# Kernel tuning notes

Measured on AMD Instinct MI355X. Metric: run time of the kernel, lower is better.

Reference implementation:

```python
import jax, jax.numpy as jnp
import numpy as np

K_NEIGHBOURS = 40  # includes self; self is dropped after top-k


def setup_inputs() -> dict:
    key = jax.random.key(0)
    ks = jax.random.split(key, 4)
    B, V, F_in = 4, 4096, 64
    P, S, F_out = 64, 4, 64
    x = jax.random.normal(ks[0], (B, V, F_in), dtype=jnp.float32)
    Wf = jax.random.normal(ks[1], (F_in, P), dtype=jnp.float32) / np.sqrt(F_in)
    bf = jnp.zeros((P,), dtype=jnp.float32)
    Ws = jax.random.normal(ks[2], (F_in, S), dtype=jnp.float32) / np.sqrt(F_in)
    bs = jnp.zeros((S,), dtype=jnp.float32)
    Wo = jax.random.normal(ks[3], (F_in + 2 * P, F_out), dtype=jnp.float32) / np.sqrt(F_in + 2 * P)
    bo = jnpp = jnp.zeros((F_out,), dtype=jnp.float32)
    return {"x": x, "Wf": Wf, "bf": bf, "Ws": Ws, "bs": bs, "Wo": Wo, "bo": bo}


def _euclidean_squared(c):
    # c: [B, V, S] -> [B, V, V] squared pairwise distances
    sq = jnp.sum(c * c, axis=-1)  # [B, V]
    d2 = sq[:, :, None] + sq[:, None, :] - 2.0 * jnp.einsum('bvs,bus->bvu', c, c)
    return d2


def reference(x, Wf, bf, Ws, bs, Wo, bo):
    # learned spatial coordinates and propagated features
    coords = x @ Ws + bs            # [B, V, S]
    feats = x @ Wf + bf             # [B, V, P]

    d2 = _euclidean_squared(coords)                 # [B, V, V]
    neg_vals, idx = jax.lax.top_k(-d2, K_NEIGHBOURS)  # closest first (self at 0)
    nbr_idx = idx[:, :, 1:]                         # [B, V, K-1]
    dist = -neg_vals[:, :, 1:]                      # [B, V, K-1] (>= 0)

    # gauss_of_lin(d * 10) = exp(-|10 d|)
    w = jnp.exp(-jnp.abs(dist * 10.0))              # [B, V, K-1]

    # gather neighbour features per batch: [B, V, K-1, P]
    nf = jax.vmap(lambda f, i: f[i])(feats, nbr_idx)
    nf = nf * w[..., None]

    collected = jnp.concatenate([jnp.max(nf, axis=2), jnp.mean(nf, axis=2)], axis=-1)  # [B, V, 2P]
    updated = jnp.concatenate([x, collected], axis=-1)  # [B, V, F_in + 2P]
    return jnp.tanh(updated @ Wo + bo)
```

## Files before the change

### kernel.cpp

```cpp
#include <hip/hip_runtime.h>
#include <cmath>

#define BB  4
#define VV  4096
#define KK  40
#define FIN 64

typedef float v2f __attribute__((ext_vector_type(2)));

__global__ __launch_bounds__(256) void prep_kernel(
    const float* __restrict__ x, const float* __restrict__ Wf,
    const float* __restrict__ bf, const float* __restrict__ Ws,
    const float* __restrict__ bs,
    float* __restrict__ coords, float* __restrict__ sq,
    float* __restrict__ feats)
{
    int lane = threadIdx.x & 63;
    int wid  = threadIdx.x >> 6;
    int row0 = (blockIdx.x * 4 + wid) * 4;
    const float* xr = x + (size_t)row0 * FIN;

    float rx0 = xr[lane];
    float rx1 = xr[64  + lane];
    float rx2 = xr[128 + lane];
    float rx3 = xr[192 + lane];

    float a0 = 0.f, a1 = 0.f, a2 = 0.f, a3 = 0.f;
    #pragma unroll
    for (int k = 0; k < FIN; ++k) {
        float wf = Wf[k * 64 + lane];
        a0 = fmaf(__uint_as_float(
             __builtin_amdgcn_readlane(__float_as_uint(rx0), k)), wf, a0);
        a1 = fmaf(__uint_as_float(
             __builtin_amdgcn_readlane(__float_as_uint(rx1), k)), wf, a1);
        a2 = fmaf(__uint_as_float(
             __builtin_amdgcn_readlane(__float_as_uint(rx2), k)), wf, a2);
        a3 = fmaf(__uint_as_float(
             __builtin_amdgcn_readlane(__float_as_uint(rx3), k)), wf, a3);
    }
    float bfl = bf[lane];
    feats[(size_t)(row0 + 0) * 64 + lane] = a0 + bfl;
    feats[(size_t)(row0 + 1) * 64 + lane] = a1 + bfl;
    feats[(size_t)(row0 + 2) * 64 + lane] = a2 + bfl;
    feats[(size_t)(row0 + 3) * 64 + lane] = a3 + bfl;

    int r  = lane >> 4;
    int s  = (lane >> 2) & 3;
    int kc = lane & 3;
    const float* xrr = x + (size_t)(row0 + r) * FIN + kc * 16;
    const float* wsr = Ws + kc * 16 * 4 + s;
    float c = 0.f;
    #pragma unroll
    for (int k = 0; k < 16; ++k)
        c = fmaf(xrr[k], wsr[k * 4], c);
    c += __shfl_xor(c, 1, 64);
    c += __shfl_xor(c, 2, 64);
    float val = c + bs[s];
    if ((lane & 3) == 0) coords[(size_t)(row0 + r) * 4 + s] = val;
    float p = val * val;
    p += __shfl_xor(p, 4, 64);
    p += __shfl_xor(p, 8, 64);
    if ((lane & 15) == 0) sq[row0 + r] = p;
}

__device__ __forceinline__ unsigned umed3(unsigned a, unsigned b, unsigned c)
{
    unsigned d;
    asm("v_med3_u32 %0, %1, %2, %3" : "=v"(d) : "v"(a), "v"(b), "v"(c));
    return d;
}

__device__ __forceinline__ int cnt_lt4(unsigned m0, unsigned m1,
                                       unsigned m2, unsigned m3,
                                       unsigned cand)
{
    return (int)__popcll(__ballot(m0 < cand))
         + (int)__popcll(__ballot(m1 < cand))
         + (int)__popcll(__ballot(m2 < cand))
         + (int)__popcll(__ballot(m3 < cand));
}

__device__ __forceinline__ unsigned select_thresh(unsigned m0, unsigned m1,
                                                  unsigned m2, unsigned m3)
{
    unsigned M = 0u;
    #pragma unroll
    for (int bit = 30; bit >= 12; --bit) {
        unsigned cand = M | (1u << bit);
        if (cnt_lt4(m0, m1, m2, m3, cand) <= 39) M = cand;
    }
    unsigned Msel = M | 0xFFFu;
    if (cnt_lt4(m0, m1, m2, m3, M + 4096u) != 40) {
        #pragma unroll
        for (int bit = 11; bit >= 0; --bit) {
            unsigned cand = M | (1u << bit);
            if (cnt_lt4(m0, m1, m2, m3, cand) <= 39) M = cand;
        }
        Msel = M;
    }
    return Msel;
}

__device__ __forceinline__ void compact4(unsigned m0, unsigned m1,
                                         unsigned m2, unsigned m3,
                                         unsigned Msel, uint2* dst)
{
    unsigned mn = m0;
    #pragma unroll
    for (int off = 32; off >= 1; off >>= 1) {
        unsigned o = __shfl_xor(mn, off, 64);
        mn = o < mn ? o : mn;
    }
    int base = 0;
    unsigned kk = m0;
    #pragma unroll
    for (int i = 0; i < 4; ++i) {
        bool pred = (kk <= Msel) && (kk != mn);
        unsigned long long mask = __ballot(pred);
        unsigned pos = (unsigned)base +
            __builtin_amdgcn_mbcnt_hi((unsigned)(mask >> 32),
                __builtin_amdgcn_mbcnt_lo((unsigned)mask, 0u));
        if (pred) {
            float d2a = __uint_as_float(kk & 0xFFFFF000u);
            float w   = __expf(-10.f * d2a);
            dst[pos] = make_uint2((kk & 4095u) << 8, __float_as_uint(w));
        }
        base += (int)__popcll(mask);
        kk = (i == 0) ? m1 : (i == 1) ? m2 : m3;
    }
}

__global__ __launch_bounds__(256) void gravnet_kernel(
    const float* __restrict__ x, const float* __restrict__ coords,
    const float* __restrict__ sq, const float* __restrict__ feats,
    const float* __restrict__ Wo, const float* __restrict__ bo,
    float* __restrict__ out)
{
    int lane = threadIdx.x & 63;
    int w    = threadIdx.x >> 6;
    int quad = w >> 1;
    int half = w & 1;
    int qb   = blockIdx.x * 8 + quad * 4;
    int b    = (blockIdx.x * 8) >> 12;
    int v0   = qb & (VV - 1);

    __shared__ __align__(16) char smem[16384];
    uint4* s_mrg = (uint4*)smem;
    uint2* s_nb  = (uint2*)smem;
    float* s_upd = (float*)(smem + 8 * KK * 8);

    const float4* cb  = (const float4*)(coords + (size_t)b * VV * 4);
    const float*  sqb = sq + (size_t)b * VV;

    float4 cq0 = cb[v0],     cq1 = cb[v0 + 1];
    float4 cq2 = cb[v0 + 2], cq3 = cb[v0 + 3];
    v2f nxA = (v2f){-2.f * cq0.x, -2.f * cq1.x};
    v2f nyA = (v2f){-2.f * cq0.y, -2.f * cq1.y};
    v2f nzA = (v2f){-2.f * cq0.z, -2.f * cq1.z};
    v2f nwA = (v2f){-2.f * cq0.w, -2.f * cq1.w};
    v2f hsA = (v2f){sqb[v0], sqb[v0 + 1]};
    v2f nxB = (v2f){-2.f * cq2.x, -2.f * cq3.x};
    v2f nyB = (v2f){-2.f * cq2.y, -2.f * cq3.y};
    v2f nzB = (v2f){-2.f * cq2.z, -2.f * cq3.z};
    v2f nwB = (v2f){-2.f * cq2.w, -2.f * cq3.w};
    v2f hsB = (v2f){sqb[v0 + 2], sqb[v0 + 3]};

    unsigned k00 = ~0u, k01 = ~0u, k02 = ~0u, k03 = ~0u;
    unsigned k10 = ~0u, k11 = ~0u, k12 = ~0u, k13 = ~0u;
    unsigned k20 = ~0u, k21 = ~0u, k22 = ~0u, k23 = ~0u;
    unsigned k30 = ~0u, k31 = ~0u, k32 = ~0u, k33 = ~0u;

    int i0 = half * 32;
    #pragma unroll 4
    for (int i = i0; i < i0 + 32; ++i) {
        int u = i * 64 + lane;
        float4 cu = cb[u];
        float squ = sqb[u];
        v2f accA = hsA + (v2f){squ, squ};
        accA = __builtin_elementwise_fma(nxA, (v2f){cu.x, cu.x}, accA);
        accA = __builtin_elementwise_fma(nyA, (v2f){cu.y, cu.y}, accA);
        accA = __builtin_elementwise_fma(nzA, (v2f){cu.z, cu.z}, accA);
        accA = __builtin_elementwise_fma(nwA, (v2f){cu.w, cu.w}, accA);
        v2f accB = hsB + (v2f){squ, squ};
        accB = __builtin_elementwise_fma(nxB, (v2f){cu.x, cu.x}, accB);
        accB = __builtin_elementwise_fma(nyB, (v2f){cu.y, cu.y}, accB);
        accB = __builtin_elementwise_fma(nzB, (v2f){cu.z, cu.z}, accB);
        accB = __builtin_elementwise_fma(nwB, (v2f){cu.w, cu.w}, accB);

        {
            float d2 = fmaxf(accA.x, 0.f);
            unsigned k = (__float_as_uint(d2) & 0xFFFFF000u) | (unsigned)u;
            unsigned n1 = umed3(k00, k01, k);
            unsigned n2 = umed3(k01, k02, k);
            unsigned n3 = umed3(k02, k03, k);
            k00 = min(k00, k); k01 = n1; k02 = n2; k03 = n3;
        }
        {
            float d2 = fmaxf(accA.y, 0.f);
            unsigned k = (__float_as_uint(d2) & 0xFFFFF000u) | (unsigned)u;
            unsigned n1 = umed3(k10, k11, k);
            unsigned n2 = umed3(k11, k12, k);
            unsigned n3 = umed3(k12, k13, k);
            k10 = min(k10, k); k11 = n1; k12 = n2; k13 = n3;
        }
        {
            float d2 = fmaxf(accB.x, 0.f);
            unsigned k = (__float_as_uint(d2) & 0xFFFFF000u) | (unsigned)u;
            unsigned n1 = umed3(k20, k21, k);
            unsigned n2 = umed3(k21, k22, k);
            unsigned n3 = umed3(k22, k23, k);
            k20 = min(k20, k); k21 = n1; k22 = n2; k23 = n3;
        }
        {
            float d2 = fmaxf(accB.y, 0.f);
            unsigned k = (__float_as_uint(d2) & 0xFFFFF000u) | (unsigned)u;
            unsigned n1 = umed3(k30, k31, k);
            unsigned n2 = umed3(k31, k32, k);
            unsigned n3 = umed3(k32, k33, k);
            k30 = min(k30, k); k31 = n1; k32 = n2; k33 = n3;
        }
    }

    s_mrg[(w * 4 + 0) * 64 + lane] = make_uint4(k00, k01, k02, k03);
    s_mrg[(w * 4 + 1) * 64 + lane] = make_uint4(k10, k11, k12, k13);
    s_mrg[(w * 4 + 2) * 64 + lane] = make_uint4(k20, k21, k22, k23);
    s_mrg[(w * 4 + 3) * 64 + lane] = make_uint4(k30, k31, k32, k33);
    __syncthreads();

    int p   = w ^ 1;
    int lq0 = half * 2;
    uint4 pb0 = s_mrg[(p * 4 + lq0)     * 64 + lane];
    uint4 pb1 = s_mrg[(p * 4 + lq0 + 1) * 64 + lane];
    unsigned oa0 = half ? k20 : k00, oa1 = half ? k21 : k01;
    unsigned oa2 = half ? k22 : k02, oa3 = half ? k23 : k03;
    unsigned ob0 = half ? k30 : k10, ob1 = half ? k31 : k11;
    unsigned ob2 = half ? k32 : k12, ob3 = half ? k33 : k13;
    __syncthreads();

    unsigned d0 = min(oa0, pb0.w), d1 = min(oa1, pb0.z);
    unsigned d2 = min(oa2, pb0.y), d3 = min(oa3, pb0.x);
    unsigned A0 = min(d0, d3), A3 = max(d0, d3);
    unsigned e0 = min(ob0, pb1.w), e1 = min(ob1, pb1.z);
    unsigned e2 = min(ob2, pb1.y), e3 = min(ob3, pb1.x);
    unsigned B0 = min(e0, e3), B3 = max(e0, e3);

    int s0 = w * 2, s1 = w * 2 + 1;
    compact4(A0, d1, d2, A3, select_thresh(A0, d1, d2, A3), &s_nb[s0 * KK]);
    compact4(B0, e1, e2, B3, select_thresh(B0, e1, e2, B3), &s_nb[s1 * KK]);

    const float* fb  = feats + (size_t)b * VV * 64;
    const char*  fbl = (const char*)(fb + lane);
    float vmax0 = -INFINITY, vsum0 = 0.f, vmax1 = -INFINITY, vsum1 = 0.f;
    #pragma unroll 6
    for (int j = 0; j < KK - 1; ++j) {
        uint2 n0 = s_nb[s0 * KK + j];
        uint2 n1 = s_nb[s1 * KK + j];
        float f0 = *(const float*)(fbl + n0.x);
        float f1 = *(const float*)(fbl + n1.x);
        float g0 = __uint_as_float(n0.y) * f0;
        float g1 = __uint_as_float(n1.y) * f1;
        vmax0 = fmaxf(vmax0, g0); vsum0 += g0;
        vmax1 = fmaxf(vmax1, g1); vsum1 += g1;
    }

    int q0g = qb + lq0, q1g = qb + lq0 + 1;
    s_upd[s0 * 192 + lane]       = x[(size_t)q0g * 64 + lane];
    s_upd[s0 * 192 + 64  + lane] = vmax0;
    s_upd[s0 * 192 + 128 + lane] = vsum0 * (1.0f / 39.0f);
    s_upd[s1 * 192 + lane]       = x[(size_t)q1g * 64 + lane];
    s_upd[s1 * 192 + 64  + lane] = vmax1;
    s_upd[s1 * 192 + 128 + lane] = vsum1 * (1.0f / 39.0f);

    float bol = bo[lane];
    float acc0 = bol, acc1 = bol;
    #pragma unroll 4
    for (int j4 = 0; j4 < 48; ++j4) {
        float wo0 = Wo[(j4 * 4 + 0) * 64 + lane];
        float wo1 = Wo[(j4 * 4 + 1) * 64 + lane];
        float wo2 = Wo[(j4 * 4 + 2) * 64 + lane];
        float wo3 = Wo[(j4 * 4 + 3) * 64 + lane];
        float4 u0 = *(const float4*)&s_upd[s0 * 192 + j4 * 4];
        float4 u1 = *(const float4*)&s_upd[s1 * 192 + j4 * 4];
        acc0 = fmaf(u0.x, wo0, acc0);  acc1 = fmaf(u1.x, wo0, acc1);
        acc0 = fmaf(u0.y, wo1, acc0);  acc1 = fmaf(u1.y, wo1, acc1);
        acc0 = fmaf(u0.z, wo2, acc0);  acc1 = fmaf(u1.z, wo2, acc1);
        acc0 = fmaf(u0.w, wo3, acc0);  acc1 = fmaf(u1.w, wo3, acc1);
    }
    float e0t = __expf(2.f * acc0);
    float e1t = __expf(2.f * acc1);
    out[(size_t)q0g * 64 + lane] = 1.f - __fdividef(2.f, e0t + 1.f);
    out[(size_t)q1g * 64 + lane] = 1.f - __fdividef(2.f, e1t + 1.f);
}

extern "C" void kernel_launch(void* const* d_in, const int* in_sizes, int n_in,
                              void* d_out, int out_size, void* d_ws, size_t ws_size,
                              hipStream_t stream)
{
    (void)in_sizes; (void)n_in; (void)out_size; (void)ws_size;
    const float* x  = (const float*)d_in[0];
    const float* Wf = (const float*)d_in[1];
    const float* bf = (const float*)d_in[2];
    const float* Ws = (const float*)d_in[3];
    const float* bs = (const float*)d_in[4];
    const float* Wo = (const float*)d_in[5];
    const float* bo = (const float*)d_in[6];
    float* out = (float*)d_out;

    float* coords = (float*)d_ws;
    float* sq     = coords + (size_t)BB * VV * 4;
    float* feats  = sq + (size_t)BB * VV;

    prep_kernel<<<BB * VV / 16, 256, 0, stream>>>(x, Wf, bf, Ws, bs,
                                                  coords, sq, feats);
    gravnet_kernel<<<BB * VV / 8, 256, 0, stream>>>(x, coords, sq, feats,
                                                    Wo, bo, out);
}
```

Before: 119.9 us.

## Swizzle block order, use v_bfi keys, and pack aggregation/output matmul into v2f

Remaps blockIdx so consecutive blocks are spread across batch/vertex ranges with an XCD-style stride of eight. Builds the distance|index sort key with a single v_bfi_b32 instead of an and/or pair. Vectorises the neighbour max/sum and the output projection into packed two-lane float math, storing the x/max/mean inputs interleaved per query pair so one float4 LDS read feeds two packed FMAs. These changes aim to cut VALU instruction count and improve cache locality, at the cost of extra register packing and a changed LDS layout.

```diff
diff --git a/kernel.cpp b/kernel.cpp
--- a/kernel.cpp
+++ b/kernel.cpp
@@ -70,6 +70,14 @@
     return d;
 }
 
+__device__ __forceinline__ unsigned bfi_key(unsigned maskv, unsigned d2b,
+                                            unsigned u)
+{
+    unsigned d;
+    asm("v_bfi_b32 %0, %1, %2, %3" : "=v"(d) : "v"(maskv), "v"(d2b), "v"(u));
+    return d;
+}
+
 __device__ __forceinline__ int cnt_lt4(unsigned m0, unsigned m1,
                                        unsigned m2, unsigned m3,
                                        unsigned cand)
@@ -140,8 +148,9 @@
     int w    = threadIdx.x >> 6;
     int quad = w >> 1;
     int half = w & 1;
-    int qb   = blockIdx.x * 8 + quad * 4;
-    int b    = (blockIdx.x * 8) >> 12;
+    int bid  = (int)((blockIdx.x & 7) * 256 + (blockIdx.x >> 3));
+    int qb   = bid * 8 + quad * 4;
+    int b    = (bid * 8) >> 12;
     int v0   = qb & (VV - 1);
 
     __shared__ __align__(16) char smem[16384];
@@ -169,6 +178,8 @@
     unsigned k10 = ~0u, k11 = ~0u, k12 = ~0u, k13 = ~0u;
     unsigned k20 = ~0u, k21 = ~0u, k22 = ~0u, k23 = ~0u;
     unsigned k30 = ~0u, k31 = ~0u, k32 = ~0u, k33 = ~0u;
+
+    unsigned maskv = 0xFFFFF000u;
 
     int i0 = half * 32;
     #pragma unroll 4
@@ -189,7 +200,7 @@
 
         {
             float d2 = fmaxf(accA.x, 0.f);
-            unsigned k = (__float_as_uint(d2) & 0xFFFFF000u) | (unsigned)u;
+            unsigned k = bfi_key(maskv, __float_as_uint(d2), (unsigned)u);
             unsigned n1 = umed3(k00, k01, k);
             unsigned n2 = umed3(k01, k02, k);
             unsigned n3 = umed3(k02, k03, k);
@@ -197,7 +208,7 @@
         }
         {
             float d2 = fmaxf(accA.y, 0.f);
-            unsigned k = (__float_as_uint(d2) & 0xFFFFF000u) | (unsigned)u;
+            unsigned k = bfi_key(maskv, __float_as_uint(d2), (unsigned)u);
             unsigned n1 = umed3(k10, k11, k);
             unsigned n2 = umed3(k11, k12, k);
             unsigned n3 = umed3(k12, k13, k);
@@ -205,7 +216,7 @@
         }
         {
             float d2 = fmaxf(accB.x, 0.f);
-            unsigned k = (__float_as_uint(d2) & 0xFFFFF000u) | (unsigned)u;
+            unsigned k = bfi_key(maskv, __float_as_uint(d2), (unsigned)u);
             unsigned n1 = umed3(k20, k21, k);
             unsigned n2 = umed3(k21, k22, k);
             unsigned n3 = umed3(k22, k23, k);
@@ -213,7 +224,7 @@
         }
         {
             float d2 = fmaxf(accB.y, 0.f);
-            unsigned k = (__float_as_uint(d2) & 0xFFFFF000u) | (unsigned)u;
+            unsigned k = bfi_key(maskv, __float_as_uint(d2), (unsigned)u);
             unsigned n1 = umed3(k30, k31, k);
             unsigned n2 = umed3(k31, k32, k);
             unsigned n3 = umed3(k32, k33, k);
@@ -250,44 +261,42 @@
 
     const float* fb  = feats + (size_t)b * VV * 64;
     const char*  fbl = (const char*)(fb + lane);
-    float vmax0 = -INFINITY, vsum0 = 0.f, vmax1 = -INFINITY, vsum1 = 0.f;
+    v2f vmax01 = (v2f){-INFINITY, -INFINITY};
+    v2f vsum01 = (v2f){0.f, 0.f};
     #pragma unroll 6
     for (int j = 0; j < KK - 1; ++j) {
         uint2 n0 = s_nb[s0 * KK + j];
         uint2 n1 = s_nb[s1 * KK + j];
         float f0 = *(const float*)(fbl + n0.x);
         float f1 = *(const float*)(fbl + n1.x);
-        float g0 = __uint_as_float(n0.y) * f0;
-        float g1 = __uint_as_float(n1.y) * f1;
-        vmax0 = fmaxf(vmax0, g0); vsum0 += g0;
-        vmax1 = fmaxf(vmax1, g1); vsum1 += g1;
+        v2f g01 = (v2f){f0, f1} *
+                  (v2f){__uint_as_float(n0.y), __uint_as_float(n1.y)};
+        vmax01 = __builtin_elementwise_max(vmax01, g01);
+        vsum01 += g01;
     }
 
     int q0g = qb + lq0, q1g = qb + lq0 + 1;
-    s_upd[s0 * 192 + lane]       = x[(size_t)q0g * 64 + lane];
-    s_upd[s0 * 192 + 64  + lane] = vmax0;
-    s_upd[s0 * 192 + 128 + lane] = vsum0 * (1.0f / 39.0f);
-    s_upd[s1 * 192 + lane]       = x[(size_t)q1g * 64 + lane];
-    s_upd[s1 * 192 + 64  + lane] = vmax1;
-    s_upd[s1 * 192 + 128 + lane] = vsum1 * (1.0f / 39.0f);
+    float* sb = s_upd + w * 384;
+    *(float2*)&sb[lane * 2] =
+        make_float2(x[(size_t)q0g * 64 + lane], x[(size_t)q1g * 64 + lane]);
+    *(float2*)&sb[128 + lane * 2] = make_float2(vmax01.x, vmax01.y);
+    *(float2*)&sb[256 + lane * 2] =
+        make_float2(vsum01.x * (1.0f / 39.0f), vsum01.y * (1.0f / 39.0f));
 
     float bol = bo[lane];
-    float acc0 = bol, acc1 = bol;
-    #pragma unroll 4
-    for (int j4 = 0; j4 < 48; ++j4) {
-        float wo0 = Wo[(j4 * 4 + 0) * 64 + lane];
-        float wo1 = Wo[(j4 * 4 + 1) * 64 + lane];
-        float wo2 = Wo[(j4 * 4 + 2) * 64 + lane];
-        float wo3 = Wo[(j4 * 4 + 3) * 64 + lane];
-        float4 u0 = *(const float4*)&s_upd[s0 * 192 + j4 * 4];
-        float4 u1 = *(const float4*)&s_upd[s1 * 192 + j4 * 4];
-        acc0 = fmaf(u0.x, wo0, acc0);  acc1 = fmaf(u1.x, wo0, acc1);
-        acc0 = fmaf(u0.y, wo1, acc0);  acc1 = fmaf(u1.y, wo1, acc1);
-        acc0 = fmaf(u0.z, wo2, acc0);  acc1 = fmaf(u1.z, wo2, acc1);
-        acc0 = fmaf(u0.w, wo3, acc0);  acc1 = fmaf(u1.w, wo3, acc1);
-    }
-    float e0t = __expf(2.f * acc0);
-    float e1t = __expf(2.f * acc1);
+    v2f acc01 = (v2f){bol, bol};
+    #pragma unroll 8
+    for (int jj = 0; jj < 96; ++jj) {
+        float wo0 = Wo[(jj * 2 + 0) * 64 + lane];
+        float wo1 = Wo[(jj * 2 + 1) * 64 + lane];
+        float4 up = *(const float4*)&sb[jj * 4];
+        acc01 = __builtin_elementwise_fma((v2f){up.x, up.y},
+                                          (v2f){wo0, wo0}, acc01);
+        acc01 = __builtin_elementwise_fma((v2f){up.z, up.w},
+                                          (v2f){wo1, wo1}, acc01);
+    }
+    float e0t = __expf(2.f * acc01.x);
+    float e1t = __expf(2.f * acc01.y);
     out[(size_t)q0g * 64 + lane] = 1.f - __fdividef(2.f, e0t + 1.f);
     out[(size_t)q1g * 64 + lane] = 1.f - __fdividef(2.f, e1t + 1.f);
 }
```

Measured after the change: 117.3 us. 1.02x faster.
